# Kernel tuning notes

Hardware: AMD Instinct MI355X
Metric: run time of the kernel (lower is better)

Reference implementation:

```python
import jax, jax.numpy as jnp
import numpy as np

B, IMG, C = 128, 128, 3
NP = 8                      # n_patches per side
PS = IMG // NP              # patch size = 16
IN_D = C * PS * PS          # 768
E, NH, L, A = 768, 12, 12, 256
HS = E // NH                # 64
T = NP * NP + 1             # 65 tokens (cls + patches)
LN_EPS = 1e-5


def _pos_emb(seq_len, d):
    i = np.arange(seq_len, dtype=np.float64)[:, None]
    j = np.arange(d, dtype=np.float64)[None, :]
    even = np.sin(i / 10000 ** (j / d))
    odd = np.cos(i / 10000 ** ((j - 1) / d))
    return jnp.asarray(np.where(j % 2 == 0, even, odd), dtype=jnp.float32)


def setup_inputs() -> dict:
    key = jax.random.key(0)
    ks = jax.random.split(key, 16)
    s_e = 1.0 / np.sqrt(E)
    s_in = 1.0 / np.sqrt(IN_D)
    s_4e = 1.0 / np.sqrt(4 * E)
    return {
        "images": jax.random.normal(ks[0], (B, IMG, IMG, C), jnp.float32),
        "lin_w": jax.random.normal(ks[1], (IN_D, E), jnp.float32) * s_in,
        "cls_tok": jax.random.uniform(ks[2], (1, E), jnp.float32),
        "pos_emb": _pos_emb(T, E),
        "Wq": jax.random.normal(ks[3], (L, E, E), jnp.float32) * s_e,
        "Wk": jax.random.normal(ks[4], (L, E, E), jnp.float32) * s_e,
        "Wv": jax.random.normal(ks[5], (L, E, E), jnp.float32) * s_e,
        "Wo": jax.random.normal(ks[6], (L, E, E), jnp.float32) * s_e,
        "bo": jnp.zeros((L, E), jnp.float32),
        "ln1g": jnp.ones((L, E), jnp.float32),
        "ln1b": jnp.zeros((L, E), jnp.float32),
        "ln2g": jnp.ones((L, E), jnp.float32),
        "ln2b": jnp.zeros((L, E), jnp.float32),
        "W1": jax.random.normal(ks[7], (L, E, 4 * E), jnp.float32) * s_e,
        "b1": jnp.zeros((L, 4 * E), jnp.float32),
        "W2": jax.random.normal(ks[8], (L, 4 * E, E), jnp.float32) * s_4e,
        "b2": jnp.zeros((L, E), jnp.float32),
        "head_w": jax.random.normal(ks[9], (E, A), jnp.float32) * s_e,
        "head_b": jnp.zeros((A,), jnp.float32),
    }


def _layernorm(x, g, b):
    mu = jnp.mean(x, axis=-1, keepdims=True)
    var = jnp.var(x, axis=-1, keepdims=True)
    return (x - mu) * jax.lax.rsqrt(var + LN_EPS) * g + b


def _vit_forward(images, lin_w, cls_tok, pos_emb, Wq, Wk, Wv, Wo, bo,
                 ln1g, ln1b, ln2g, ln2b, W1, b1, W2, b2, head_w, head_b):
    n = images.shape[0]
    # patches: 'b (h p1) (w p2) c -> b (h w) (p1 p2 c)'
    p = images.reshape(n, NP, PS, NP, PS, C)
    patches = p.transpose(0, 1, 3, 2, 4, 5).reshape(n, NP * NP, IN_D)
    x = patches @ lin_w                                   # [B, 64, E]
    x = jnp.concatenate([jnp.broadcast_to(cls_tok, (n, 1, E)), x], axis=1)
    x = x + pos_emb[None]                                 # [B, T, E]

    scale = E ** (-0.5)  # NOTE: original scales by n_embd, not head_size

    def block(x, params):
        wq, wk, wv, wo_, bo_, g1, be1, g2, be2, w1, bb1, w2, bb2 = params
        h = _layernorm(x, g1, be1)
        q = (h @ wq).reshape(n, T, NH, HS)
        k = (h @ wk).reshape(n, T, NH, HS)
        v = (h @ wv).reshape(n, T, NH, HS)
        wei = jnp.einsum('bthd,bshd->bhts', q, k) * scale
        wei = jax.nn.softmax(wei, axis=-1)
        attn = jnp.einsum('bhts,bshd->bthd', wei, v).reshape(n, T, E)
        x = x + attn @ wo_ + bo_
        h2 = _layernorm(x, g2, be2)
        x = x + jax.nn.relu(h2 @ w1 + bb1) @ w2 + bb2
        return x, None

    x, _ = jax.lax.scan(block, x,
                        (Wq, Wk, Wv, Wo, bo, ln1g, ln1b, ln2g, ln2b,
                         W1, b1, W2, b2))
    cls = x[:, 0]                                          # [B, E]
    logits = jax.nn.softmax(cls @ head_w + head_b, axis=-1)  # model ends in Softmax
    return logits


def reference(images, lin_w, cls_tok, pos_emb, Wq, Wk, Wv, Wo, bo,
              ln1g, ln1b, ln2g, ln2b, W1, b1, W2, b2, head_w, head_b):
    return _vit_forward(images, lin_w, cls_tok, pos_emb, Wq, Wk, Wv, Wo, bo,
                        ln1g, ln1b, ln2g, ln2b, W1, b1, W2, b2, head_w, head_b)
```

## Files before the change

### kernel.cpp

```cpp
#include <hip/hip_runtime.h>
#include <cstdint>
#include <cstddef>


typedef __bf16 bf16x8 __attribute__((ext_vector_type(8)));
typedef float  f32x4  __attribute__((ext_vector_type(4)));

#define DEVINL __device__ __forceinline__

DEVINL uint16_t f2bf(float f){
  union U{float f; uint32_t i;} v; v.f=f; uint32_t u=v.i;
  return (uint16_t)((u + 0x7fffu + ((u>>16)&1u)) >> 16);
}

DEVINL void gl_lds16(const void* g, void* l){
  __builtin_amdgcn_global_load_lds((const __attribute__((address_space(1))) void*)g,
                                   (__attribute__((address_space(3))) void*)l, 16, 0, 0);
}

__global__ __launch_bounds__(256) void patchify_k(const float* __restrict__ img,
                                                  uint16_t* __restrict__ out){
  int i = blockIdx.x*256 + threadIdx.x;
  int m  = i / 768, kk = i - m*768;
  int b  = m >> 6,  t  = m & 63;
  int py = t >> 3,  px = t & 7;
  int r  = kk / 48, rem = kk - r*48;
  size_t src = ((size_t)(b*128 + py*16 + r)*128 + px*16)*3 + rem;
  out[i] = f2bf(img[src]);
}

DEVINL void tile_transpose(const float* __restrict__ src, uint16_t* __restrict__ dst,
                           int R, int C, int ti, int tj, int tid){
  __shared__ uint16_t tile[32][33];
  int tx = tid & 31, ty = tid >> 5;
  int r0 = ti*32, c0 = tj*32;
  #pragma unroll
  for (int i=0;i<4;++i)
    tile[ty+i*8][tx] = f2bf(src[(size_t)(r0+ty+i*8)*C + c0 + tx]);
  __syncthreads();
  #pragma unroll
  for (int i=0;i<4;++i)
    dst[(size_t)(c0+ty+i*8)*R + r0 + tx] = tile[tx][ty+i*8];
}

__global__ __launch_bounds__(256) void transpose_cvt_k(const float* __restrict__ src,
                                                       uint16_t* __restrict__ dst, int R, int C){
  tile_transpose(src, dst, R, C, blockIdx.y, blockIdx.x, threadIdx.x);
}

__global__ __launch_bounds__(256) void prep_layer_k(
    const float* __restrict__ Wq, const float* __restrict__ Wk,
    const float* __restrict__ Wv, const float* __restrict__ Wo,
    const float* __restrict__ W1, const float* __restrict__ W2,
    uint16_t* __restrict__ wbuf){
  int idx = blockIdx.x;
  const float* src; uint16_t* dst; int R, C, ti, tj;
  if (idx < 2304){
    int m = idx / 576, t = idx - m*576; ti = t/24; tj = t - ti*24; R=768; C=768;
    src = (m==0)?Wq:(m==1)?Wk:(m==2)?Wv:Wo;
    dst = wbuf + (size_t)m*589824;
  } else if (idx < 4608){
    int t = idx - 2304; ti = t/96; tj = t - ti*96; R=768; C=3072;
    src = W1; dst = wbuf + 2359296;
  } else {
    int t = idx - 4608; ti = t/24; tj = t - ti*24; R=3072; C=768;
    src = W2; dst = wbuf + 4718592;
  }
  tile_transpose(src, dst, R, C, ti, tj, threadIdx.x);
}

__global__ __launch_bounds__(256) void cls_init_k(const float* __restrict__ ct,
                                                  const float* __restrict__ pos,
                                                  float* __restrict__ X){
  int b = blockIdx.x, tid = threadIdx.x;
  for (int e = tid; e < 768; e += 256)
    X[(size_t)b*65*768 + e] = ct[e] + pos[e];
}

__global__ __launch_bounds__(256) void ln_k(const float* __restrict__ Xin,
                                            uint16_t* __restrict__ H,
                                            const float* __restrict__ g,
                                            const float* __restrict__ b){
  int row = blockIdx.x, tid = threadIdx.x;
  const float* xr = Xin + (size_t)row*768;
  float v0 = xr[tid], v1 = xr[tid+256], v2 = xr[tid+512];
  int wid = tid>>6, lane = tid&63;
  __shared__ float part[4];
  __shared__ float bc[2];
  float s = v0+v1+v2;
  #pragma unroll
  for (int o=32;o;o>>=1) s += __shfl_down(s,o);
  if (lane==0) part[wid] = s;
  __syncthreads();
  if (tid==0) bc[0] = (part[0]+part[1]+part[2]+part[3]) * (1.f/768.f);
  __syncthreads();
  float mu = bc[0];
  float d0=v0-mu, d1=v1-mu, d2=v2-mu;
  float q = d0*d0 + d1*d1 + d2*d2;
  #pragma unroll
  for (int o=32;o;o>>=1) q += __shfl_down(q,o);
  __syncthreads();
  if (lane==0) part[wid] = q;
  __syncthreads();
  if (tid==0) bc[1] = rsqrtf((part[0]+part[1]+part[2]+part[3])*(1.f/768.f) + 1e-5f);
  __syncthreads();
  float rs = bc[1];
  uint16_t* hr = H + (size_t)row*768;
  hr[tid]     = f2bf(d0*rs*g[tid]     + b[tid]);
  hr[tid+256] = f2bf(d1*rs*g[tid+256] + b[tid+256]);
  hr[tid+512] = f2bf(d2*rs*g[tid+512] + b[tid+512]);
}

enum { EP_BF16=0, EP_RES=1, EP_RELU=2, EP_EMB=3 };

template<int MODE>
__global__ __launch_bounds__(256) void gemm_bt_k(
    const uint16_t* __restrict__ A, const uint16_t* __restrict__ Bt,
    int M, int N, int K, int strideB, long long strideO,
    const float* __restrict__ bias, float* __restrict__ X,
    uint16_t* __restrict__ Obf, const float* __restrict__ pos)
{
  __shared__ __align__(16) uint16_t sA[2][128*32];
  __shared__ __align__(16) uint16_t sB[2][128*32];
  const int tid = threadIdx.x;
  const int wid = tid>>6, lane = tid&63;
  const int bn = blockIdx.x*128, bm = blockIdx.y*128;
  const int z = blockIdx.z;
  const uint16_t* Bz = Bt + (size_t)z*strideB;
  const int wr = wid>>1, wc = wid&1;
  const int frow = lane&15, g = lane>>4;
  int srow[2], schunk[2];
  #pragma unroll
  for (int rr=0; rr<2; ++rr){
    int G = rr*256 + tid;
    srow[rr]   = G>>2;
    schunk[rr] = ((G&3) - (srow[rr]>>1)) & 3;
  }
  const int rsw = (frow>>1)&3;
  f32x4 acc[4][4] = {};
  const int nt = K>>5;

  #pragma unroll
  for (int rr=0; rr<2; ++rr){
    gl_lds16(A  + (size_t)(bm+srow[rr])*K + schunk[rr]*8,
             (char*)sA[0] + (rr*256 + wid*64)*16);
    gl_lds16(Bz + (size_t)(bn+srow[rr])*K + schunk[rr]*8,
             (char*)sB[0] + (rr*256 + wid*64)*16);
  }

  int buf = 0;
  for (int t = 0; t < nt; ++t){
    if (t+1 < nt){
      int k0 = (t+1)<<5;
      #pragma unroll
      for (int rr=0; rr<2; ++rr){
        gl_lds16(A  + (size_t)(bm+srow[rr])*K + k0 + schunk[rr]*8,
                 (char*)sA[buf^1] + (rr*256 + wid*64)*16);
        gl_lds16(Bz + (size_t)(bn+srow[rr])*K + k0 + schunk[rr]*8,
                 (char*)sB[buf^1] + (rr*256 + wid*64)*16);
      }
      asm volatile("s_waitcnt vmcnt(4)" ::: "memory");
    } else {
      asm volatile("s_waitcnt vmcnt(0)" ::: "memory");
    }
    __builtin_amdgcn_s_barrier();
    bf16x8 a[4], b[4];
    const char* sAc = (const char*)sA[buf];
    const char* sBc = (const char*)sB[buf];
    #pragma unroll
    for (int m=0;m<4;++m)
      a[m] = *(const bf16x8*)(sAc + (wr*64+m*16+frow)*64 + (((g+rsw)&3)<<4));
    #pragma unroll
    for (int n=0;n<4;++n)
      b[n] = *(const bf16x8*)(sBc + (wc*64+n*16+frow)*64 + (((g+rsw)&3)<<4));
    #pragma unroll
    for (int m=0;m<4;++m)
      #pragma unroll
      for (int n=0;n<4;++n)
        acc[m][n] = __builtin_amdgcn_mfma_f32_16x16x32_bf16(a[m], b[n], acc[m][n], 0,0,0);
    __builtin_amdgcn_s_barrier();
    buf ^= 1;
  }

  uint16_t* Oz = Obf + (size_t)z*(size_t)strideO;
  #pragma unroll
  for (int m=0;m<4;++m){
    int gr0 = bm + wr*64 + m*16 + (lane>>4)*4;
    #pragma unroll
    for (int n=0;n<4;++n){
      int gc = bn + wc*64 + n*16 + (lane&15);
      #pragma unroll
      for (int r=0;r<4;++r){
        int grow = gr0 + r;
        float vsum = acc[m][n][r];
        if constexpr (MODE==EP_BF16){
          Oz[(size_t)grow*N + gc] = f2bf(vsum);
        } else if constexpr (MODE==EP_RES){
          X[(size_t)grow*N + gc] += vsum + bias[gc];
        } else if constexpr (MODE==EP_RELU){
          float u = vsum + bias[gc];
          Oz[(size_t)grow*N + gc] = f2bf(u > 0.f ? u : 0.f);
        } else {
          int t2 = grow & 63, bb = grow >> 6;
          X[((size_t)bb*65 + 1 + t2)*768 + gc] = vsum + pos[(size_t)(t2+1)*768 + gc];
        }
      }
    }
  }
}

__global__ __launch_bounds__(320) void attn_mfma_k(const uint16_t* __restrict__ q,
    const uint16_t* __restrict__ k, const uint16_t* __restrict__ v,
    uint16_t* __restrict__ o)
{
  __shared__ __align__(16) uint16_t P_lds[80][104];
  __shared__ __align__(16) uint16_t Vt[64][104];
  const int bh = blockIdx.x; const int b = bh / 12, hd = bh - b*12;
  const int tid = threadIdx.x;
  const int m = tid>>6;
  const int lane = tid&63;
  const int g = lane>>4, c = lane&15;
  const size_t base = (size_t)b*65*768 + (size_t)hd*64;

  for (int i = tid; i < 80*16; i += 320) P_lds[i>>4][80 + (i&15)] = 0;
  for (int i = tid; i < 64*32; i += 320) Vt[i>>5][64 + (i&31)] = 0;
  __syncthreads();
  for (int j = tid; j < 520; j += 320){
    int key = j >> 3, dc = j & 7;
    union { bf16x8 v8; uint16_t u[8]; } gv;
    gv.v8 = *(const bf16x8*)&v[base + (size_t)key*768 + dc*8];
    #pragma unroll
    for (int e = 0; e < 8; ++e) Vt[dc*8 + e][key] = gv.u[e];
  }

  bf16x8 bk[5][2];
  #pragma unroll
  for (int n=0;n<5;++n)
    #pragma unroll
    for (int kk=0;kk<2;++kk)
      bk[n][kk] = *(const bf16x8*)&k[base + (size_t)(n*16 + c)*768 + kk*32 + g*8];

  bf16x8 aq[2];
  #pragma unroll
  for (int kk=0;kk<2;++kk)
    aq[kk] = *(const bf16x8*)&q[base + (size_t)(m*16 + c)*768 + kk*32 + g*8];
  f32x4 sacc[5] = {};
  #pragma unroll
  for (int kk=0;kk<2;++kk)
    #pragma unroll
    for (int n=0;n<5;++n)
      sacc[n] = __builtin_amdgcn_mfma_f32_16x16x32_bf16(aq[kk], bk[n][kk], sacc[n], 0,0,0);

  const float scale = 0.03608439182435161f;
  #pragma unroll
  for (int r=0;r<4;++r){
    float val[5]; float mx = -3.0e38f;
    #pragma unroll
    for (int n=0;n<5;++n){
      val[n] = (n*16 + c) < 65 ? sacc[n][r]*scale : -3.0e38f;
      mx = fmaxf(mx, val[n]);
    }
    #pragma unroll
    for (int off=1; off<16; off<<=1) mx = fmaxf(mx, __shfl_xor(mx, off));
    float p[5], sum = 0.f;
    #pragma unroll
    for (int n=0;n<5;++n){
      p[n] = (n*16 + c) < 65 ? __expf(val[n]-mx) : 0.f;
      sum += p[n];
    }
    #pragma unroll
    for (int off=1; off<16; off<<=1) sum += __shfl_xor(sum, off);
    float rinv = 1.f / sum;
    int row = m*16 + g*4 + r;
    #pragma unroll
    for (int n=0;n<5;++n) P_lds[row][n*16 + c] = f2bf(p[n]*rinv);
  }
  __syncthreads();

  bf16x8 vb[4][3];
  #pragma unroll
  for (int n=0;n<4;++n)
    #pragma unroll
    for (int kk=0;kk<3;++kk)
      vb[n][kk] = *(const bf16x8*)&Vt[n*16 + c][kk*32 + g*8];
  f32x4 oacc[4] = {};
  #pragma unroll
  for (int kk=0;kk<3;++kk){
    bf16x8 pa = *(const bf16x8*)&P_lds[m*16 + c][kk*32 + g*8];
    #pragma unroll
    for (int n=0;n<4;++n)
      oacc[n] = __builtin_amdgcn_mfma_f32_16x16x32_bf16(pa, vb[n][kk], oacc[n], 0,0,0);
  }
  #pragma unroll
  for (int r=0;r<4;++r){
    int row = m*16 + g*4 + r;
    if (row < 65){
      #pragma unroll
      for (int n=0;n<4;++n)
        o[base + (size_t)row*768 + n*16 + c] = f2bf(oacc[n][r]);
    }
  }
}

__global__ __launch_bounds__(256) void head_k(const float* __restrict__ X,
    const float* __restrict__ W, const float* __restrict__ bias,
    float* __restrict__ out){
  int b = blockIdx.x, a = threadIdx.x;
  const float* xr = X + (size_t)b*65*768;
  float acc = bias[a];
  for (int kk=0; kk<768; ++kk) acc += xr[kk]*W[(size_t)kk*256 + a];
  int wid = a>>6, lane = a&63;
  __shared__ float red[4];
  float mx = acc;
  #pragma unroll
  for (int off=32; off; off>>=1) mx = fmaxf(mx, __shfl_xor(mx, off));
  if (lane==0) red[wid]=mx;
  __syncthreads();
  mx = fmaxf(fmaxf(red[0],red[1]), fmaxf(red[2],red[3]));
  float e = __expf(acc-mx);
  float s = e;
  #pragma unroll
  for (int off=32; off; off>>=1) s += __shfl_xor(s, off);
  __syncthreads();
  if (lane==0) red[wid]=s;
  __syncthreads();
  s = red[0]+red[1]+red[2]+red[3];
  out[(size_t)b*256 + a] = e/s;
}

extern "C" void kernel_launch(void* const* d_in, const int* in_sizes, int n_in,
                              void* d_out, int out_size, void* d_ws, size_t ws_size,
                              hipStream_t stream)
{
  const float* images = (const float*)d_in[0];
  const float* lin_w  = (const float*)d_in[1];
  const float* cls_tok= (const float*)d_in[2];
  const float* pos    = (const float*)d_in[3];
  const float* Wq = (const float*)d_in[4];
  const float* Wk = (const float*)d_in[5];
  const float* Wv = (const float*)d_in[6];
  const float* Wo = (const float*)d_in[7];
  const float* bo = (const float*)d_in[8];
  const float* ln1g=(const float*)d_in[9];
  const float* ln1b=(const float*)d_in[10];
  const float* ln2g=(const float*)d_in[11];
  const float* ln2b=(const float*)d_in[12];
  const float* W1 = (const float*)d_in[13];
  const float* b1 = (const float*)d_in[14];
  const float* W2 = (const float*)d_in[15];
  const float* b2 = (const float*)d_in[16];
  const float* hw = (const float*)d_in[17];
  const float* hb = (const float*)d_in[18];

  char* ws = (char*)d_ws;
  float*    x    = (float*)   (ws + 0);
  uint16_t* h    = (uint16_t*)(ws + 25559040);
  uint16_t* qkv  = (uint16_t*)(ws + 38338560);
  uint16_t* attn = (uint16_t*)(ws + 76677120);
  uint16_t* mid  = (uint16_t*)(ws + 89456640);
  uint16_t* wbuf = (uint16_t*)(ws + 140574720);
  uint16_t* lwt  = (uint16_t*)(ws + 154730496);

  patchify_k<<<24576,256,0,stream>>>(images, mid);
  transpose_cvt_k<<<dim3(24,24),256,0,stream>>>(lin_w, lwt, 768, 768);
  gemm_bt_k<EP_EMB><<<dim3(6,64,1),256,0,stream>>>(mid, lwt, 8192,768,768, 0,0,
                                                   nullptr, x, nullptr, pos);
  cls_init_k<<<128,256,0,stream>>>(cls_tok, pos, x);

  for (int l=0;l<12;++l){
    prep_layer_k<<<6912,256,0,stream>>>(Wq+(size_t)l*589824, Wk+(size_t)l*589824,
                                        Wv+(size_t)l*589824, Wo+(size_t)l*589824,
                                        W1+(size_t)l*2359296, W2+(size_t)l*2359296, wbuf);
    ln_k<<<8320,256,0,stream>>>(x, h, ln1g+(size_t)l*768, ln1b+(size_t)l*768);
    gemm_bt_k<EP_BF16><<<dim3(6,65,3),256,0,stream>>>(h, wbuf, 8320,768,768,
                                                      589824, 6389760LL,
                                                      nullptr, nullptr, qkv, nullptr);
    attn_mfma_k<<<1536,320,0,stream>>>(qkv, qkv+6389760, qkv+12779520, attn);
    gemm_bt_k<EP_RES><<<dim3(6,65,1),256,0,stream>>>(attn, wbuf+1769472, 8320,768,768,
                                                     0,0, bo+(size_t)l*768, x, nullptr, nullptr);
    ln_k<<<8320,256,0,stream>>>(x, h, ln2g+(size_t)l*768, ln2b+(size_t)l*768);
    gemm_bt_k<EP_RELU><<<dim3(24,65,1),256,0,stream>>>(h, wbuf+2359296, 8320,3072,768,
                                                       0,0, b1+(size_t)l*3072, nullptr, mid, nullptr);
    gemm_bt_k<EP_RES><<<dim3(6,65,1),256,0,stream>>>(mid, wbuf+4718592, 8320,768,3072,
                                                     0,0, b2+(size_t)l*768, x, nullptr, nullptr);
  }
  head_k<<<128,256,0,stream>>>(x, hw, hb, (float*)d_out);
}
```

Baseline: 3.551 ms.

## Template GEMM on N-tile width and add XCD-aware block swizzle

Makes the GEMM tile width a template parameter and uses 128x64 tiles for the N=768 projections (embedding, Wo, W2), doubling their grid to fill the MI355X's CUs better. It also remaps workgroup indices so that consecutive tiles land on the same XCD, improving L2 reuse of shared A and B panels. Narrower tiles mean less data reuse per loaded A tile and fewer MFMAs per barrier, and the wait count is adjusted for the smaller number of B loads.

After: 3.268 ms. -8.0%, faster.

```diff
diff --git a/kernel.cpp b/kernel.cpp
--- a/kernel.cpp
+++ b/kernel.cpp
@@ -113,70 +113,86 @@
 
 enum { EP_BF16=0, EP_RES=1, EP_RELU=2, EP_EMB=3 };
 
-template<int MODE>
+template<int MODE, int BN>
 __global__ __launch_bounds__(256) void gemm_bt_k(
     const uint16_t* __restrict__ A, const uint16_t* __restrict__ Bt,
     int M, int N, int K, int strideB, long long strideO,
     const float* __restrict__ bias, float* __restrict__ X,
     uint16_t* __restrict__ Obf, const float* __restrict__ pos)
 {
+  constexpr int WN = BN/2;
+  constexpr int NF = WN/16;
+  constexpr int BLOADS = BN/64;
   __shared__ __align__(16) uint16_t sA[2][128*32];
-  __shared__ __align__(16) uint16_t sB[2][128*32];
+  __shared__ __align__(16) uint16_t sB[2][BN*32];
   const int tid = threadIdx.x;
   const int wid = tid>>6, lane = tid&63;
-  const int bn = blockIdx.x*128, bm = blockIdx.y*128;
+  const int nx = gridDim.x;
+  const int nwg = nx*gridDim.y;
+  {
+  }
+  int idx = blockIdx.y*nx + blockIdx.x;
+  int q8 = nwg>>3, r8 = nwg&7, xcd = idx&7, off = idx>>3;
+  int swz = (xcd<r8 ? xcd*(q8+1) : r8*(q8+1) + (xcd-r8)*q8) + off;
+  const int bn = (swz % nx)*BN, bm = (swz / nx)*128;
   const int z = blockIdx.z;
   const uint16_t* Bz = Bt + (size_t)z*strideB;
   const int wr = wid>>1, wc = wid&1;
   const int frow = lane&15, g = lane>>4;
-  int srow[2], schunk[2];
+  int srA[2], scA[2];
   #pragma unroll
   for (int rr=0; rr<2; ++rr){
     int G = rr*256 + tid;
-    srow[rr]   = G>>2;
-    schunk[rr] = ((G&3) - (srow[rr]>>1)) & 3;
+    srA[rr] = G>>2; scA[rr] = ((G&3) - (G>>3)) & 3;
+  }
+  int srB[2], scB[2];
+  #pragma unroll
+  for (int rr=0; rr<BLOADS; ++rr){
+    int G = rr*256 + tid;
+    srB[rr] = G>>2; scB[rr] = ((G&3) - (G>>3)) & 3;
   }
   const int rsw = (frow>>1)&3;
-  f32x4 acc[4][4] = {};
+  f32x4 acc[4][NF] = {};
   const int nt = K>>5;
 
   #pragma unroll
-  for (int rr=0; rr<2; ++rr){
-    gl_lds16(A  + (size_t)(bm+srow[rr])*K + schunk[rr]*8,
-             (char*)sA[0] + (rr*256 + wid*64)*16);
-    gl_lds16(Bz + (size_t)(bn+srow[rr])*K + schunk[rr]*8,
-             (char*)sB[0] + (rr*256 + wid*64)*16);
-  }
+  for (int rr=0; rr<2; ++rr)
+    gl_lds16(A + (size_t)(bm+srA[rr])*K + scA[rr]*8, (char*)sA[0] + (rr*256 + wid*64)*16);
+  #pragma unroll
+  for (int rr=0; rr<BLOADS; ++rr)
+    gl_lds16(Bz + (size_t)(bn+srB[rr])*K + scB[rr]*8, (char*)sB[0] + (rr*256 + wid*64)*16);
 
   int buf = 0;
   for (int t = 0; t < nt; ++t){
     if (t+1 < nt){
       int k0 = (t+1)<<5;
       #pragma unroll
-      for (int rr=0; rr<2; ++rr){
-        gl_lds16(A  + (size_t)(bm+srow[rr])*K + k0 + schunk[rr]*8,
+      for (int rr=0; rr<2; ++rr)
+        gl_lds16(A + (size_t)(bm+srA[rr])*K + k0 + scA[rr]*8,
                  (char*)sA[buf^1] + (rr*256 + wid*64)*16);
-        gl_lds16(Bz + (size_t)(bn+srow[rr])*K + k0 + schunk[rr]*8,
+      #pragma unroll
+      for (int rr=0; rr<BLOADS; ++rr)
+        gl_lds16(Bz + (size_t)(bn+srB[rr])*K + k0 + scB[rr]*8,
                  (char*)sB[buf^1] + (rr*256 + wid*64)*16);
-      }
-      asm volatile("s_waitcnt vmcnt(4)" ::: "memory");
+      if constexpr (BLOADS==1) asm volatile("s_waitcnt vmcnt(3)" ::: "memory");
+      else                     asm volatile("s_waitcnt vmcnt(4)" ::: "memory");
     } else {
       asm volatile("s_waitcnt vmcnt(0)" ::: "memory");
     }
     __builtin_amdgcn_s_barrier();
-    bf16x8 a[4], b[4];
+    bf16x8 a[4], b[NF];
     const char* sAc = (const char*)sA[buf];
     const char* sBc = (const char*)sB[buf];
     #pragma unroll
     for (int m=0;m<4;++m)
       a[m] = *(const bf16x8*)(sAc + (wr*64+m*16+frow)*64 + (((g+rsw)&3)<<4));
     #pragma unroll
-    for (int n=0;n<4;++n)
-      b[n] = *(const bf16x8*)(sBc + (wc*64+n*16+frow)*64 + (((g+rsw)&3)<<4));
+    for (int n=0;n<NF;++n)
+      b[n] = *(const bf16x8*)(sBc + (wc*WN+n*16+frow)*64 + (((g+rsw)&3)<<4));
     #pragma unroll
     for (int m=0;m<4;++m)
       #pragma unroll
-      for (int n=0;n<4;++n)
+      for (int n=0;n<NF;++n)
         acc[m][n] = __builtin_amdgcn_mfma_f32_16x16x32_bf16(a[m], b[n], acc[m][n], 0,0,0);
     __builtin_amdgcn_s_barrier();
     buf ^= 1;
@@ -187,8 +203,8 @@
   for (int m=0;m<4;++m){
     int gr0 = bm + wr*64 + m*16 + (lane>>4)*4;
     #pragma unroll
-    for (int n=0;n<4;++n){
-      int gc = bn + wc*64 + n*16 + (lane&15);
+    for (int n=0;n<NF;++n){
+      int gc = bn + wc*WN + n*16 + (lane&15);
       #pragma unroll
       for (int r=0;r<4;++r){
         int grow = gr0 + r;
@@ -363,7 +379,7 @@
 
   patchify_k<<<24576,256,0,stream>>>(images, mid);
   transpose_cvt_k<<<dim3(24,24),256,0,stream>>>(lin_w, lwt, 768, 768);
-  gemm_bt_k<EP_EMB><<<dim3(6,64,1),256,0,stream>>>(mid, lwt, 8192,768,768, 0,0,
+  gemm_bt_k<EP_EMB,64><<<dim3(12,64,1),256,0,stream>>>(mid, lwt, 8192,768,768, 0,0,
                                                    nullptr, x, nullptr, pos);
   cls_init_k<<<128,256,0,stream>>>(cls_tok, pos, x);
 
@@ -372,16 +388,16 @@
                                         Wv+(size_t)l*589824, Wo+(size_t)l*589824,
                                         W1+(size_t)l*2359296, W2+(size_t)l*2359296, wbuf);
     ln_k<<<8320,256,0,stream>>>(x, h, ln1g+(size_t)l*768, ln1b+(size_t)l*768);
-    gemm_bt_k<EP_BF16><<<dim3(6,65,3),256,0,stream>>>(h, wbuf, 8320,768,768,
+    gemm_bt_k<EP_BF16,128><<<dim3(6,65,3),256,0,stream>>>(h, wbuf, 8320,768,768,
                                                       589824, 6389760LL,
                                                       nullptr, nullptr, qkv, nullptr);
     attn_mfma_k<<<1536,320,0,stream>>>(qkv, qkv+6389760, qkv+12779520, attn);
-    gemm_bt_k<EP_RES><<<dim3(6,65,1),256,0,stream>>>(attn, wbuf+1769472, 8320,768,768,
+    gemm_bt_k<EP_RES,64><<<dim3(12,65,1),256,0,stream>>>(attn, wbuf+1769472, 8320,768,768,
                                                      0,0, bo+(size_t)l*768, x, nullptr, nullptr);
     ln_k<<<8320,256,0,stream>>>(x, h, ln2g+(size_t)l*768, ln2b+(size_t)l*768);
-    gemm_bt_k<EP_RELU><<<dim3(24,65,1),256,0,stream>>>(h, wbuf+2359296, 8320,3072,768,
+    gemm_bt_k<EP_RELU,128><<<dim3(24,65,1),256,0,stream>>>(h, wbuf+2359296, 8320,3072,768,
                                                        0,0, b1+(size_t)l*3072, nullptr, mid, nullptr);
-    gemm_bt_k<EP_RES><<<dim3(6,65,1),256,0,stream>>>(mid, wbuf+4718592, 8320,768,3072,
+    gemm_bt_k<EP_RES,64><<<dim3(12,65,1),256,0,stream>>>(mid, wbuf+4718592, 8320,768,3072,
                                                      0,0, b2+(size_t)l*768, x, nullptr, nullptr);
   }
   head_k<<<128,256,0,stream>>>(x, hw, hb, (float*)d_out);
```
